# Kernel optimization log

Measured on AMD Instinct MI355X. Metric: run time of the kernel, lower is better.

Reference implementation:

```python
import jax, jax.numpy as jnp
import numpy as np

NGRAM = 2
NUM_HEADS = 16
NUM_BUCKETS = 32
EMBED_DIM = 1024
REAL_T = 512
BSZ = 4


def setup_inputs() -> dict:
    key = jax.random.key(0)
    ks = jax.random.split(key, 10)
    tgt_len = (1 + NGRAM) * REAL_T
    E, H, NB = EMBED_DIM, NUM_HEADS, NUM_BUCKETS
    w = 0.02
    return {
        "query": jax.random.normal(ks[0], (tgt_len, BSZ, E), jnp.float32),
        "self_attn_mask": jnp.zeros((REAL_T, REAL_T), jnp.float32),
        "ngram_mask_matrix": jnp.zeros((NGRAM, REAL_T, 2 * REAL_T), jnp.float32),
        "i_buckets_main_stream": jax.random.randint(ks[1], (BSZ, REAL_T, REAL_T), 0, NB, jnp.int32),
        "i_bucket_relative_stream": jax.random.randint(ks[2], (BSZ, REAL_T, 2 * REAL_T), 0, NB, jnp.int32),
        "in_proj_weight": jax.random.normal(ks[3], (3 * E, E), jnp.float32) * w,
        "in_proj_bias": jnp.zeros((3 * E,), jnp.float32),
        "out_proj_weight": jax.random.normal(ks[4], (E, E), jnp.float32) * w,
        "out_proj_bias": jnp.zeros((E,), jnp.float32),
        "relative_weight": jax.random.normal(ks[5], (NB * H, E), jnp.float32) * w,
        "relative_bias": jnp.zeros((NB * H,), jnp.float32),
    }


def _forward(query, self_attn_mask, ngram_mask_matrix,
             ib_main, ib_rel,
             in_proj_weight, in_proj_bias, out_proj_weight, out_proj_bias,
             relative_weight, relative_bias):
    tgt_len, bsz, E = query.shape
    H, n = NUM_HEADS, NGRAM
    hd = E // H
    nb = relative_weight.shape[0] // H
    T = tgt_len // (1 + n)
    scaling = hd ** -0.5

    # fused qkv projection
    qkv = query @ in_proj_weight.T + in_proj_bias  # [tgt, B, 3E]
    q, k, v = jnp.split(qkv, 3, axis=-1)
    q = q * scaling

    def to_bh(x):  # [tgt, B, E] -> [B*H, tgt, hd]
        return x.reshape(tgt_len, bsz * H, hd).transpose(1, 0, 2)
    q, k, v = to_bh(q), to_bh(k), to_bh(v)

    h_main = query[:T]                                  # [T, B, E]
    h_pred = query[T:].reshape(n, T, bsz, E)            # [n, T, B, E]
    q_main, k_main, v_main = q[:, :T], k[:, :T], v[:, :T]            # [BH, T, hd]
    def pred(x):  # [BH, n*T, hd] -> [n, BH, T, hd]
        return x[:, T:].reshape(bsz * H, n, T, hd).transpose(1, 0, 2, 3)
    q_pred, k_pred, v_pred = pred(q), pred(k), pred(v)

    # ---- main stream ----
    aw_main = jnp.einsum('bth,bsh->bts', q_main, k_main)  # [BH, T, T]
    # relative bias: per-token bucket values gathered by bucket index
    vals_main = h_main.transpose(1, 0, 2) @ relative_weight.T + relative_bias  # [B, T, nb*H]
    vals_main = vals_main.reshape(bsz, T, nb, H).transpose(0, 3, 1, 2)         # [B, H, T, nb]
    ib = jnp.broadcast_to(ib_main[:, None].astype(jnp.int32), (bsz, H, T, T))
    rel_main = jnp.take_along_axis(vals_main, ib, axis=-1).reshape(bsz * H, T, T)
    aw_main = aw_main + rel_main + self_attn_mask[None]
    p_main = jax.nn.softmax(aw_main, axis=-1)
    attn_main = jnp.einsum('bts,bsh->bth', p_main, v_main)  # [BH, T, hd]
    attn_main = attn_main.transpose(1, 0, 2).reshape(T, bsz, E)

    # ---- ngram predict streams ----
    k_ng = jnp.concatenate([jnp.broadcast_to(k_main[None], (n,) + k_main.shape), k_pred], axis=2)  # [n, BH, 2T, hd]
    v_ng = jnp.concatenate([jnp.broadcast_to(v_main[None], (n,) + v_main.shape), v_pred], axis=2)
    aw_ng = jnp.einsum('nbtc,nbsc->nbts', q_pred, k_ng)  # [n, BH, T, 2T]

    vals_ng = h_pred.transpose(0, 2, 1, 3) @ relative_weight.T + relative_bias  # [n, B, T, nb*H]
    vals_ng = vals_ng.reshape(n, bsz, T, nb, H).transpose(0, 1, 4, 2, 3)        # [n, B, H, T, nb]
    ibr = jnp.broadcast_to(ib_rel[None, :, None].astype(jnp.int32), (n, bsz, H, T, 2 * T))
    rel_ng = jnp.take_along_axis(vals_ng, ibr, axis=-1).reshape(n, bsz * H, T, 2 * T)
    aw_ng = aw_ng + rel_ng + ngram_mask_matrix[:, None]
    p_ng = jax.nn.softmax(aw_ng, axis=-1)
    attn_ng = jnp.einsum('nbts,nbsc->nbtc', p_ng, v_ng)  # [n, BH, T, hd]
    attn_ng = attn_ng.transpose(0, 2, 1, 3).reshape(n * T, bsz, E)

    attn = jnp.concatenate([attn_main, attn_ng], axis=0)  # [tgt, B, E]
    return attn @ out_proj_weight.T + out_proj_bias


def reference(query, self_attn_mask, ngram_mask_matrix,
              i_buckets_main_stream, i_bucket_relative_stream,
              in_proj_weight, in_proj_bias, out_proj_weight, out_proj_bias,
              relative_weight, relative_bias):
    return _forward(query, self_attn_mask, ngram_mask_matrix,
                    i_buckets_main_stream, i_bucket_relative_stream,
                    in_proj_weight, in_proj_bias, out_proj_weight, out_proj_bias,
                    relative_weight, relative_bias)
```

## Files before the change

### kernel.cpp

```cpp
#include <hip/hip_runtime.h>

#define TSEQ 512
#define BSZN 4
#define NH 16
#define NBN 32
#define EMB 1024
#define HD 64
#define TGT 1536
#define MROWS 6144

typedef unsigned short ushort_t;
typedef __bf16 bf8 __attribute__((ext_vector_type(8)));
typedef ushort_t u16x8v __attribute__((ext_vector_type(8)));
typedef float f32x4 __attribute__((ext_vector_type(4)));

__device__ __forceinline__ unsigned short f2bf(float f) {
  unsigned int u = __builtin_bit_cast(unsigned int, f);
  u += 0x7fffu + ((u >> 16) & 1u);
  return (unsigned short)(u >> 16);
}

__device__ __forceinline__ float bf2f(unsigned short u) {
  return __builtin_bit_cast(float, (unsigned int)u << 16);
}

__device__ __forceinline__ unsigned int packbf(float a, float b) {
  return (unsigned int)f2bf(a) | ((unsigned int)f2bf(b) << 16);
}

__device__ __forceinline__ void gload16(const void* g, void* l) {
  __builtin_amdgcn_global_load_lds(
      (const __attribute__((address_space(1))) void*)g,
      (__attribute__((address_space(3))) void*)l, 16, 0, 0);
}

__device__ __forceinline__ f32x4 mfma_bf16(bf8 a, bf8 b, f32x4 c) {
  return __builtin_amdgcn_mfma_f32_16x16x32_bf16(a, b, c, 0, 0, 0);
}

__device__ __forceinline__ float lanebcast(float v, int srclane) {
  return __builtin_bit_cast(float,
      __builtin_amdgcn_ds_bpermute(srclane * 4, __builtin_bit_cast(int, v)));
}

__global__ void cvt4_kernel(const float* __restrict__ q, const float* __restrict__ win,
                            const float* __restrict__ wout, const float* __restrict__ wrel,
                            ushort_t* __restrict__ qo, ushort_t* __restrict__ wino,
                            ushort_t* __restrict__ wouto, ushort_t* __restrict__ wrelo) {
  const int i = blockIdx.x * blockDim.x + threadIdx.x;
  const int n0 = 1572864, n1 = 786432, n2 = 262144, n3 = 131072;
  const float* src;
  ushort_t* dst;
  int off;
  if (i < n0) { src = q; dst = qo; off = i; }
  else if (i < n0 + n1) { src = win; dst = wino; off = i - n0; }
  else if (i < n0 + n1 + n2) { src = wout; dst = wouto; off = i - n0 - n1; }
  else if (i < n0 + n1 + n2 + n3) { src = wrel; dst = wrelo; off = i - n0 - n1 - n2; }
  else return;
  const float4 v = reinterpret_cast<const float4*>(src)[off];
  ushort4 o;
  o.x = f2bf(v.x); o.y = f2bf(v.y); o.z = f2bf(v.z); o.w = f2bf(v.w);
  reinterpret_cast<ushort4*>(dst)[off] = o;
}

__global__ void prep_comb_kernel(const int* __restrict__ ibm, const int* __restrict__ ibr,
                                 const float* __restrict__ mm, const float* __restrict__ mng,
                                 unsigned int* __restrict__ cm, unsigned int* __restrict__ cng) {
  const int i = blockIdx.x * blockDim.x + threadIdx.x;
  const int nm = 262144;
  const int nr = 1048576;
  if (i < nm) {
    const int f = i * 4;
    const int4 ib = *reinterpret_cast<const int4*>(ibm + f);
    const float4 mk = *reinterpret_cast<const float4*>(mm + (f & 262143));
    uint4 o;
    o.x = ((unsigned int)f2bf(mk.x) << 16) | ((unsigned int)ib.x & 31u);
    o.y = ((unsigned int)f2bf(mk.y) << 16) | ((unsigned int)ib.y & 31u);
    o.z = ((unsigned int)f2bf(mk.z) << 16) | ((unsigned int)ib.z & 31u);
    o.w = ((unsigned int)f2bf(mk.w) << 16) | ((unsigned int)ib.w & 31u);
    *reinterpret_cast<uint4*>(cm + f) = o;
  } else if (i < nm + nr) {
    const int f = (i - nm) * 4;
    const int ib_off = ((f >> 20) << 19) + (f & 524287);
    const int mk_off = f & 1048575;
    const int4 ib = *reinterpret_cast<const int4*>(ibr + ib_off);
    const float4 mk = *reinterpret_cast<const float4*>(mng + mk_off);
    uint4 o;
    o.x = ((unsigned int)f2bf(mk.x) << 16) | ((unsigned int)ib.x & 31u);
    o.y = ((unsigned int)f2bf(mk.y) << 16) | ((unsigned int)ib.y & 31u);
    o.z = ((unsigned int)f2bf(mk.z) << 16) | ((unsigned int)ib.z & 31u);
    o.w = ((unsigned int)f2bf(mk.w) << 16) | ((unsigned int)ib.w & 31u);
    *reinterpret_cast<uint4*>(cng + f) = o;
  }
}

template <int MODE>
__global__ __launch_bounds__(256) void gemm_bt(
    const ushort_t* __restrict__ A, const ushort_t* __restrict__ B,
    const float* __restrict__ bias, float* __restrict__ Cf,
    ushort_t* __restrict__ Qo, ushort_t* __restrict__ Ko, ushort_t* __restrict__ Vto,
    int M, int N, int K) {
  __shared__ ushort_t lds[16384];
  ushort_t* lA = lds;
  ushort_t* lB = lds + 8192;

  const int tid = threadIdx.x;
  const int lane = tid & 63;
  const int wid = tid >> 6;
  const int l15 = lane & 15, l4 = lane >> 4;
  const int bm = blockIdx.y, bn = blockIdx.x;
  const int wm = (wid >> 1) * 64, wn = (wid & 1) * 64;

  f32x4 acc[4][4] = {};

  const int r8 = tid >> 3;
  const int c8 = ((tid & 7) ^ (r8 & 7)) * 8;
  const ushort_t* Ag = A + (size_t)(bm * 128 + r8) * K + c8;
  const ushort_t* Bg = B + (size_t)(bn * 128 + r8) * K + c8;
  ushort_t* lAp = lA + tid * 8;
  ushort_t* lBp = lB + tid * 8;

  for (int kt = 0; kt < K; kt += 64) {
    __syncthreads();
#pragma unroll
    for (int i = 0; i < 4; ++i) {
      gload16(Ag + (size_t)i * 32 * K + kt, lAp + i * 2048);
      gload16(Bg + (size_t)i * 32 * K + kt, lBp + i * 2048);
    }
    __syncthreads();
#pragma unroll
    for (int k0 = 0; k0 < 2; ++k0) {
      bf8 af[4], bv[4];
#pragma unroll
      for (int mi = 0; mi < 4; ++mi) {
        const int row = wm + mi * 16 + l15;
        const int slot = (k0 * 4 + l4) ^ (row & 7);
        af[mi] = *reinterpret_cast<const bf8*>(lA + row * 64 + slot * 8);
      }
#pragma unroll
      for (int ni = 0; ni < 4; ++ni) {
        const int row = wn + ni * 16 + l15;
        const int slot = (k0 * 4 + l4) ^ (row & 7);
        bv[ni] = *reinterpret_cast<const bf8*>(lB + row * 64 + slot * 8);
      }
#pragma unroll
      for (int mi = 0; mi < 4; ++mi)
#pragma unroll
        for (int ni = 0; ni < 4; ++ni)
          acc[mi][ni] = mfma_bf16(af[mi], bv[ni], acc[mi][ni]);
    }
  }

  if (MODE == 0 && bn >= 16) {
    __syncthreads();
    char* tb = reinterpret_cast<char*>(lds);
#pragma unroll
    for (int ni = 0; ni < 4; ++ni) {
      const int colloc = wn + ni * 16 + l15;
      const float bc = bias[bn * 128 + colloc];
      const unsigned int swz = (colloc & 7) << 4;
#pragma unroll
      for (int mi = 0; mi < 4; ++mi) {
        const int t_loc = (wm >> 2) + mi * 4 + l4;
        f32x4 v = acc[mi][ni];
#pragma unroll
        for (int r = 0; r < 4; ++r) {
          const int byteoff = colloc * 256 + ((r * 64 + t_loc * 2) ^ swz);
          *reinterpret_cast<ushort_t*>(tb + byteoff) = f2bf(v[r] + bc);
        }
      }
    }
    __syncthreads();
    const int tglob0 = bm * 32;
#pragma unroll
    for (int p = 0; p < 2; ++p) {
      const int pair = wid * 2 + p;
      const int bb = pair >> 1;
      const int hl = pair & 1;
      const int hh = (bn - 16) * 2 + hl;
      const int bh = bb * NH + hh;
      const int tch = lane & 3;
#pragma unroll
      for (int ii = 0; ii < 4; ++ii) {
        const int dloc = ii * 16 + (lane >> 2);
        const int colloc = hl * 64 + dloc;
        const int byteoff = colloc * 256 + ((bb * 64 + tch * 16) ^ ((colloc & 7) << 4));
        const u16x8v val = *reinterpret_cast<const u16x8v*>(tb + byteoff);
        *reinterpret_cast<u16x8v*>(
            Vto + ((size_t)bh * HD + dloc) * TGT + tglob0 + tch * 8) = val;
      }
    }
    return;
  }

#pragma unroll
  for (int ni = 0; ni < 4; ++ni) {
    const int col = bn * 128 + wn + ni * 16 + l15;
    const float bc = bias[col];
#pragma unroll
    for (int mi = 0; mi < 4; ++mi) {
      const int row0 = bm * 128 + wm + mi * 16 + l4 * 4;
      f32x4 v = acc[mi][ni];
#pragma unroll
      for (int r = 0; r < 4; ++r) {
        const int row = row0 + r;
        float val = v[r] + bc;
        if (MODE == 0) {
          const int part = col >> 10;
          const int cc = col & 1023;
          const int h = cc >> 6, d = cc & 63;
          const int t = row >> 2, bb = row & 3;
          const int bh = bb * NH + h;
          if (part == 0) {
            Qo[((size_t)bh * TGT + t) * HD + d] = f2bf(val * 0.125f);
          } else {
            Ko[((size_t)bh * TGT + t) * HD + d] = f2bf(val);
          }
        } else if (MODE == 3) {
          const int hh = col & 15, nb = col >> 4;
          const int qg = row >> 2, bb2 = row & 3;
          Qo[(((size_t)(bb2 * NH + hh)) * TGT + qg) * NBN + nb] = f2bf(val);
        } else {
          Cf[(size_t)row * N + col] = val;
        }
      }
    }
  }
}

__global__ __launch_bounds__(256, 3) void attn_kernel(
    const ushort_t* __restrict__ Q, const ushort_t* __restrict__ Kb,
    const ushort_t* __restrict__ Vt, const ushort_t* __restrict__ VMh,
    const unsigned int* __restrict__ comb_main, const unsigned int* __restrict__ comb_ng,
    ushort_t* __restrict__ AT) {
  __shared__ unsigned char kbuf[8192];
  __shared__ unsigned char vbuf[8192];
  __shared__ ushort_t vmt[4][1024];
  __shared__ unsigned int pbl[4][1152];

  const int tid = threadIdx.x;
  const int lane = tid & 63, wid = tid >> 6;
  const int l15 = lane & 15, l4 = lane >> 4;

  const int n = blockIdx.x;
  const int xcd = n & 7;
  const int b = xcd >> 1;
  const int idx = (xcd & 1) * 96 + (n >> 3);
  const int h = idx / 12;
  const int rem = idx - h * 12;
  const int z = rem >> 2;
  const int blk = rem & 3;
  const int g = (z == 0) ? 0 : z - 1;
  const int bh = b * NH + h;
  const int t0 = blk * 128 + wid * 32;
  const int qrow0 = (z == 0) ? t0 : TSEQ + g * TSEQ + t0;
  const int nsb = (z == 0) ? 8 : 16;

  gload16(VMh + ((size_t)bh * TGT + qrow0 + (lane >> 2)) * NBN + (lane & 3) * 8,
          (ushort_t*)vmt[wid] + lane * 8);
  gload16(VMh + ((size_t)bh * TGT + qrow0 + 16 + (lane >> 2)) * NBN + (lane & 3) * 8,
          (ushort_t*)vmt[wid] + 512 + lane * 8);

  bf8 qf[2][2];
#pragma unroll
  for (int th = 0; th < 2; ++th)
#pragma unroll
    for (int hf = 0; hf < 2; ++hf)
      qf[th][hf] = *reinterpret_cast<const bf8*>(
          &Q[((size_t)bh * TGT + qrow0 + th * 16 + l15) * HD + hf * 32 + l4 * 8]);

  const unsigned int* cb[2];
  {
    const unsigned int* cbase = (z == 0)
        ? comb_main + (size_t)b * TSEQ * TSEQ
        : comb_ng + (size_t)(b * 2 + g) * TSEQ * (2 * TSEQ);
    const int sstr = (z == 0) ? TSEQ : 2 * TSEQ;
    cb[0] = cbase + (size_t)(t0 + l15) * sstr;
    cb[1] = cbase + (size_t)(t0 + 16 + l15) * sstr;
  }

  float m_run[2] = {-1e30f, -1e30f};
  float l_run[2] = {0.f, 0.f};
  f32x4 oacc[2][4] = {};

  const int r8 = lane >> 3;
  const int swzs = ((lane & 7) ^ r8) << 4;
  const int swzr = (l15 & 7) << 4;

  for (int sb = 0; sb < nsb; ++sb) {
    const int srow0 = (sb < 8) ? sb * 64 : TSEQ + g * TSEQ + (sb - 8) * 64;
    const int scol = sb * 64;

    __syncthreads();
    {
      const ushort_t* ks = Kb + ((size_t)bh * TGT + srow0 + wid * 16 + r8) * HD + (swzs >> 1);
      gload16(ks, kbuf + wid * 2048 + lane * 16);
      gload16(ks + 8 * HD, kbuf + wid * 2048 + 1024 + lane * 16);
      const ushort_t* vs = Vt + ((size_t)bh * HD + wid * 16 + r8) * TGT + srow0 + (swzs >> 1);
      gload16(vs, vbuf + wid * 2048 + lane * 16);
      gload16(vs + 8 * TGT, vbuf + wid * 2048 + 1024 + lane * 16);
    }
    __syncthreads();

    bf8 kf[4][2];
#pragma unroll
    for (int j = 0; j < 4; ++j) {
      const int row = j * 16 + l15;
      kf[j][0] = *reinterpret_cast<const bf8*>(kbuf + row * 128 + ((l4 * 16) ^ swzr));
      kf[j][1] = *reinterpret_cast<const bf8*>(kbuf + row * 128 + ((64 + l4 * 16) ^ swzr));
    }

#pragma unroll
    for (int th = 0; th < 2; ++th) {
      const unsigned int* cwp = cb[th] + scol + l4 * 4;
      const uint4 c0 = *reinterpret_cast<const uint4*>(cwp);
      const uint4 c1 = *reinterpret_cast<const uint4*>(cwp + 16);
      const uint4 c2 = *reinterpret_cast<const uint4*>(cwp + 32);
      const uint4 c3 = *reinterpret_cast<const uint4*>(cwp + 48);
      const unsigned int cwa[4][4] = {{c0.x, c0.y, c0.z, c0.w},
                                      {c1.x, c1.y, c1.z, c1.w},
                                      {c2.x, c2.y, c2.z, c2.w},
                                      {c3.x, c3.y, c3.z, c3.w}};
      f32x4 st[4];
#pragma unroll
      for (int j = 0; j < 4; ++j) {
        f32x4 s4 = {};
        s4 = mfma_bf16(kf[j][0], qf[th][0], s4);
        s4 = mfma_bf16(kf[j][1], qf[th][1], s4);
        st[j] = s4;
      }
      const ushort_t* vrow = vmt[wid] + (th * 16 + l15) * 32;
      float vals[4][4];
      float mx = -1e30f;
#pragma unroll
      for (int j = 0; j < 4; ++j) {
#pragma unroll
        for (int r = 0; r < 4; ++r) {
          const unsigned int w = cwa[j][r];
          const float v = st[j][r] + bf2f((ushort_t)(w >> 16)) + bf2f(vrow[w & 31u]);
          vals[j][r] = v;
          mx = fmaxf(mx, v);
        }
      }
      mx = fmaxf(mx, __shfl_xor(mx, 16));
      mx = fmaxf(mx, __shfl_xor(mx, 32));
      const float oldm = m_run[th];
      const float newm = fmaxf(oldm, mx);
      const float fct = (oldm <= -1e30f) ? 0.f : __expf(oldm - newm);
      float lsum = 0.f;
#pragma unroll
      for (int j = 0; j < 4; ++j) {
        const float p0 = __expf(vals[j][0] - newm);
        const float p1 = __expf(vals[j][1] - newm);
        const float p2 = __expf(vals[j][2] - newm);
        const float p3 = __expf(vals[j][3] - newm);
        lsum += (p0 + p1) + (p2 + p3);
        pbl[wid][th * 576 + l15 * 36 + j * 8 + l4 * 2 + 0] = packbf(p0, p1);
        pbl[wid][th * 576 + l15 * 36 + j * 8 + l4 * 2 + 1] = packbf(p2, p3);
      }
      lsum += __shfl_xor(lsum, 16);
      lsum += __shfl_xor(lsum, 32);
      l_run[th] = l_run[th] * fct + lsum;
      m_run[th] = newm;

      f32x4 rs;
      rs[0] = lanebcast(fct, l4 * 4 + 0);
      rs[1] = lanebcast(fct, l4 * 4 + 1);
      rs[2] = lanebcast(fct, l4 * 4 + 2);
      rs[3] = lanebcast(fct, l4 * 4 + 3);
#pragma unroll
      for (int dt = 0; dt < 4; ++dt) oacc[th][dt] *= rs;

      const ushort_t* pbase = reinterpret_cast<const ushort_t*>(&pbl[wid][th * 576]);
#pragma unroll
      for (int k32 = 0; k32 < 2; ++k32) {
        const bf8 pa = *reinterpret_cast<const bf8*>(pbase + l15 * 72 + k32 * 32 + l4 * 8);
#pragma unroll
        for (int dt = 0; dt < 4; ++dt) {
          const bf8 vb = *reinterpret_cast<const bf8*>(
              vbuf + (dt * 16 + l15) * 128 + ((k32 * 64 + l4 * 16) ^ swzr));
          oacc[th][dt] = mfma_bf16(pa, vb, oacc[th][dt]);
        }
      }
    }
  }

#pragma unroll
  for (int th = 0; th < 2; ++th) {
    const float linv = 1.f / l_run[th];
    f32x4 bs;
    bs[0] = lanebcast(linv, l4 * 4 + 0);
    bs[1] = lanebcast(linv, l4 * 4 + 1);
    bs[2] = lanebcast(linv, l4 * 4 + 2);
    bs[3] = lanebcast(linv, l4 * 4 + 3);
#pragma unroll
    for (int dt = 0; dt < 4; ++dt) {
#pragma unroll
      for (int r = 0; r < 4; ++r) {
        const int tout = qrow0 + th * 16 + l4 * 4 + r;
        AT[((size_t)tout * BSZN + b) * EMB + h * HD + dt * 16 + l15] =
            f2bf(oacc[th][dt][r] * bs[r]);
      }
    }
  }
}

extern "C" void kernel_launch(void* const* d_in, const int* in_sizes, int n_in,
                              void* d_out, int out_size, void* d_ws, size_t ws_size,
                              hipStream_t stream) {
  const float* query     = (const float*)d_in[0];
  const float* mask_main = (const float*)d_in[1];
  const float* mask_ng   = (const float*)d_in[2];
  const int*   ib_main   = (const int*)d_in[3];
  const int*   ib_rel    = (const int*)d_in[4];
  const float* w_in      = (const float*)d_in[5];
  const float* b_in      = (const float*)d_in[6];
  const float* w_out     = (const float*)d_in[7];
  const float* b_out     = (const float*)d_in[8];
  const float* w_rel     = (const float*)d_in[9];
  const float* b_rel     = (const float*)d_in[10];
  float* out = (float*)d_out;

  ushort_t* qbf    = (ushort_t*)d_ws;
  ushort_t* winbf  = qbf + 6291456;
  ushort_t* woutbf = winbf + 3145728;
  ushort_t* relwbf = woutbf + 1048576;
  ushort_t* Qb     = relwbf + 524288;
  ushort_t* Kbuf   = Qb + 6291456;
  ushort_t* Vtb    = Kbuf + 6291456;
  ushort_t* VMh    = Vtb + 6291456;
  unsigned int* comb_main = (unsigned int*)(VMh + 3145728);
  unsigned int* comb_ng   = comb_main + 1048576;
  ushort_t* AT     = qbf;

  {
    const int total4 = 1572864 + 786432 + 262144 + 131072;
    cvt4_kernel<<<(total4 + 255) / 256, 256, 0, stream>>>(query, w_in, w_out, w_rel,
                                                          qbf, winbf, woutbf, relwbf);
  }
  prep_comb_kernel<<<(262144 + 1048576) / 256, 256, 0, stream>>>(
      ib_main, ib_rel, mask_main, mask_ng, comb_main, comb_ng);

  gemm_bt<0><<<dim3(24, 48), 256, 0, stream>>>(qbf, winbf, b_in, nullptr,
                                               Qb, Kbuf, Vtb, MROWS, 3072, 1024);
  gemm_bt<3><<<dim3(4, 48), 256, 0, stream>>>(qbf, relwbf, b_rel, nullptr,
                                              VMh, nullptr, nullptr, MROWS, 512, 1024);
  attn_kernel<<<768, 256, 0, stream>>>(Qb, Kbuf, Vtb, VMh, comb_main, comb_ng, AT);
  gemm_bt<2><<<dim3(8, 48), 256, 0, stream>>>(AT, woutbf, b_out, out,
                                              nullptr, nullptr, nullptr, MROWS, 1024, 1024);
}
```

Measured before the change: 217.6 us.

## Double-buffer K/V tiles, use exp2 softmax with lazy rescale, merge prep kernels

The attention kernel now double-buffers its K/V LDS tiles, prefetching the next block while computing the current one, so each iteration needs one barrier instead of two. The log2(e) factor is folded into Q scaling, the relative-bucket values and the masks, so the softmax can use exp2f. Accumulator rescaling is skipped unless the running max rises by more than 8. The P staging buffer is shrunk and swizzled, stored with vector writes, and bf16 conversion uses native casts. The two preprocessing kernels are merged into one launch. The lazy rescale lets exponentials reach up to 2^8 before bf16 packing, which carries some accuracy risk, and the extra LDS buffers may reduce occupancy.

Measured after the change: 212.9 us. 2.1% less time.

```diff
diff --git a/kernel.cpp b/kernel.cpp
--- a/kernel.cpp
+++ b/kernel.cpp
@@ -8,16 +8,17 @@
 #define HD 64
 #define TGT 1536
 #define MROWS 6144
+#define LOG2E 1.44269504088896f
 
 typedef unsigned short ushort_t;
 typedef __bf16 bf8 __attribute__((ext_vector_type(8)));
+typedef __bf16 bf2_t __attribute__((ext_vector_type(2)));
 typedef ushort_t u16x8v __attribute__((ext_vector_type(8)));
+typedef unsigned int u32x2 __attribute__((ext_vector_type(2)));
 typedef float f32x4 __attribute__((ext_vector_type(4)));
 
 __device__ __forceinline__ unsigned short f2bf(float f) {
-  unsigned int u = __builtin_bit_cast(unsigned int, f);
-  u += 0x7fffu + ((u >> 16) & 1u);
-  return (unsigned short)(u >> 16);
+  return __builtin_bit_cast(unsigned short, (__bf16)f);
 }
 
 __device__ __forceinline__ float bf2f(unsigned short u) {
@@ -25,7 +26,10 @@
 }
 
 __device__ __forceinline__ unsigned int packbf(float a, float b) {
-  return (unsigned int)f2bf(a) | ((unsigned int)f2bf(b) << 16);
+  bf2_t t;
+  t[0] = (__bf16)a;
+  t[1] = (__bf16)b;
+  return __builtin_bit_cast(unsigned int, t);
 }
 
 __device__ __forceinline__ void gload16(const void* g, void* l) {
@@ -43,53 +47,50 @@
       __builtin_amdgcn_ds_bpermute(srclane * 4, __builtin_bit_cast(int, v)));
 }
 
-__global__ void cvt4_kernel(const float* __restrict__ q, const float* __restrict__ win,
-                            const float* __restrict__ wout, const float* __restrict__ wrel,
-                            ushort_t* __restrict__ qo, ushort_t* __restrict__ wino,
-                            ushort_t* __restrict__ wouto, ushort_t* __restrict__ wrelo) {
+__global__ void prep_all_kernel(const float* __restrict__ q, const float* __restrict__ win,
+                                const float* __restrict__ wout, const float* __restrict__ wrel,
+                                const int* __restrict__ ibm, const int* __restrict__ ibr,
+                                const float* __restrict__ mm, const float* __restrict__ mng,
+                                ushort_t* __restrict__ qo, ushort_t* __restrict__ wino,
+                                ushort_t* __restrict__ wouto, ushort_t* __restrict__ wrelo,
+                                unsigned int* __restrict__ cm, unsigned int* __restrict__ cng) {
   const int i = blockIdx.x * blockDim.x + threadIdx.x;
   const int n0 = 1572864, n1 = 786432, n2 = 262144, n3 = 131072;
-  const float* src;
-  ushort_t* dst;
-  int off;
-  if (i < n0) { src = q; dst = qo; off = i; }
-  else if (i < n0 + n1) { src = win; dst = wino; off = i - n0; }
-  else if (i < n0 + n1 + n2) { src = wout; dst = wouto; off = i - n0 - n1; }
-  else if (i < n0 + n1 + n2 + n3) { src = wrel; dst = wrelo; off = i - n0 - n1 - n2; }
-  else return;
-  const float4 v = reinterpret_cast<const float4*>(src)[off];
-  ushort4 o;
-  o.x = f2bf(v.x); o.y = f2bf(v.y); o.z = f2bf(v.z); o.w = f2bf(v.w);
-  reinterpret_cast<ushort4*>(dst)[off] = o;
-}
-
-__global__ void prep_comb_kernel(const int* __restrict__ ibm, const int* __restrict__ ibr,
-                                 const float* __restrict__ mm, const float* __restrict__ mng,
-                                 unsigned int* __restrict__ cm, unsigned int* __restrict__ cng) {
-  const int i = blockIdx.x * blockDim.x + threadIdx.x;
-  const int nm = 262144;
-  const int nr = 1048576;
-  if (i < nm) {
-    const int f = i * 4;
+  const int ncvt = n0 + n1 + n2 + n3;
+  const int nm = 262144, nr = 1048576;
+  if (i < ncvt) {
+    const float* src;
+    ushort_t* dst;
+    int off;
+    if (i < n0) { src = q; dst = qo; off = i; }
+    else if (i < n0 + n1) { src = win; dst = wino; off = i - n0; }
+    else if (i < n0 + n1 + n2) { src = wout; dst = wouto; off = i - n0 - n1; }
+    else { src = wrel; dst = wrelo; off = i - n0 - n1 - n2; }
+    const float4 v = reinterpret_cast<const float4*>(src)[off];
+    ushort4 o;
+    o.x = f2bf(v.x); o.y = f2bf(v.y); o.z = f2bf(v.z); o.w = f2bf(v.w);
+    reinterpret_cast<ushort4*>(dst)[off] = o;
+  } else if (i < ncvt + nm) {
+    const int f = (i - ncvt) * 4;
     const int4 ib = *reinterpret_cast<const int4*>(ibm + f);
     const float4 mk = *reinterpret_cast<const float4*>(mm + (f & 262143));
     uint4 o;
-    o.x = ((unsigned int)f2bf(mk.x) << 16) | ((unsigned int)ib.x & 31u);
-    o.y = ((unsigned int)f2bf(mk.y) << 16) | ((unsigned int)ib.y & 31u);
-    o.z = ((unsigned int)f2bf(mk.z) << 16) | ((unsigned int)ib.z & 31u);
-    o.w = ((unsigned int)f2bf(mk.w) << 16) | ((unsigned int)ib.w & 31u);
+    o.x = ((unsigned int)f2bf(mk.x * LOG2E) << 16) | ((unsigned int)ib.x & 31u);
+    o.y = ((unsigned int)f2bf(mk.y * LOG2E) << 16) | ((unsigned int)ib.y & 31u);
+    o.z = ((unsigned int)f2bf(mk.z * LOG2E) << 16) | ((unsigned int)ib.z & 31u);
+    o.w = ((unsigned int)f2bf(mk.w * LOG2E) << 16) | ((unsigned int)ib.w & 31u);
     *reinterpret_cast<uint4*>(cm + f) = o;
-  } else if (i < nm + nr) {
-    const int f = (i - nm) * 4;
+  } else if (i < ncvt + nm + nr) {
+    const int f = (i - ncvt - nm) * 4;
     const int ib_off = ((f >> 20) << 19) + (f & 524287);
     const int mk_off = f & 1048575;
     const int4 ib = *reinterpret_cast<const int4*>(ibr + ib_off);
     const float4 mk = *reinterpret_cast<const float4*>(mng + mk_off);
     uint4 o;
-    o.x = ((unsigned int)f2bf(mk.x) << 16) | ((unsigned int)ib.x & 31u);
-    o.y = ((unsigned int)f2bf(mk.y) << 16) | ((unsigned int)ib.y & 31u);
-    o.z = ((unsigned int)f2bf(mk.z) << 16) | ((unsigned int)ib.z & 31u);
-    o.w = ((unsigned int)f2bf(mk.w) << 16) | ((unsigned int)ib.w & 31u);
+    o.x = ((unsigned int)f2bf(mk.x * LOG2E) << 16) | ((unsigned int)ib.x & 31u);
+    o.y = ((unsigned int)f2bf(mk.y * LOG2E) << 16) | ((unsigned int)ib.y & 31u);
+    o.z = ((unsigned int)f2bf(mk.z * LOG2E) << 16) | ((unsigned int)ib.z & 31u);
+    o.w = ((unsigned int)f2bf(mk.w * LOG2E) << 16) | ((unsigned int)ib.w & 31u);
     *reinterpret_cast<uint4*>(cng + f) = o;
   }
 }
@@ -212,14 +213,14 @@
           const int t = row >> 2, bb = row & 3;
           const int bh = bb * NH + h;
           if (part == 0) {
-            Qo[((size_t)bh * TGT + t) * HD + d] = f2bf(val * 0.125f);
+            Qo[((size_t)bh * TGT + t) * HD + d] = f2bf(val * (0.125f * LOG2E));
           } else {
             Ko[((size_t)bh * TGT + t) * HD + d] = f2bf(val);
           }
         } else if (MODE == 3) {
           const int hh = col & 15, nb = col >> 4;
           const int qg = row >> 2, bb2 = row & 3;
-          Qo[(((size_t)(bb2 * NH + hh)) * TGT + qg) * NBN + nb] = f2bf(val);
+          Qo[(((size_t)(bb2 * NH + hh)) * TGT + qg) * NBN + nb] = f2bf(val * LOG2E);
         } else {
           Cf[(size_t)row * N + col] = val;
         }
@@ -233,10 +234,10 @@
     const ushort_t* __restrict__ Vt, const ushort_t* __restrict__ VMh,
     const unsigned int* __restrict__ comb_main, const unsigned int* __restrict__ comb_ng,
     ushort_t* __restrict__ AT) {
-  __shared__ unsigned char kbuf[8192];
-  __shared__ unsigned char vbuf[8192];
+  __shared__ unsigned char kbuf[2][8192];
+  __shared__ unsigned char vbuf[2][8192];
   __shared__ ushort_t vmt[4][1024];
-  __shared__ unsigned int pbl[4][1152];
+  __shared__ unsigned int pbl[4][512];
 
   const int tid = threadIdx.x;
   const int lane = tid & 63, wid = tid >> 6;
@@ -286,28 +287,36 @@
   const int r8 = lane >> 3;
   const int swzs = ((lane & 7) ^ r8) << 4;
   const int swzr = (l15 & 7) << 4;
-
+  const int swz2 = (l15 & 7) << 2;
+
+  auto stage = [&](int sb, int bf) {
+    const int srow0 = (sb < 8) ? sb * 64 : TSEQ + g * TSEQ + (sb - 8) * 64;
+    const ushort_t* ks = Kb + ((size_t)bh * TGT + srow0 + wid * 16 + r8) * HD + (swzs >> 1);
+    gload16(ks, &kbuf[bf][wid * 2048 + lane * 16]);
+    gload16(ks + 8 * HD, &kbuf[bf][wid * 2048 + 1024 + lane * 16]);
+    const ushort_t* vs = Vt + ((size_t)bh * HD + wid * 16 + r8) * TGT + srow0 + (swzs >> 1);
+    gload16(vs, &vbuf[bf][wid * 2048 + lane * 16]);
+    gload16(vs + 8 * TGT, &vbuf[bf][wid * 2048 + 1024 + lane * 16]);
+  };
+
+  stage(0, 0);
+  asm volatile("s_waitcnt vmcnt(0)" ::: "memory");
+  __builtin_amdgcn_s_barrier();
+
+  int cur = 0;
   for (int sb = 0; sb < nsb; ++sb) {
-    const int srow0 = (sb < 8) ? sb * 64 : TSEQ + g * TSEQ + (sb - 8) * 64;
     const int scol = sb * 64;
-
-    __syncthreads();
-    {
-      const ushort_t* ks = Kb + ((size_t)bh * TGT + srow0 + wid * 16 + r8) * HD + (swzs >> 1);
-      gload16(ks, kbuf + wid * 2048 + lane * 16);
-      gload16(ks + 8 * HD, kbuf + wid * 2048 + 1024 + lane * 16);
-      const ushort_t* vs = Vt + ((size_t)bh * HD + wid * 16 + r8) * TGT + srow0 + (swzs >> 1);
-      gload16(vs, vbuf + wid * 2048 + lane * 16);
-      gload16(vs + 8 * TGT, vbuf + wid * 2048 + 1024 + lane * 16);
-    }
-    __syncthreads();
+    if (sb + 1 < nsb) stage(sb + 1, cur ^ 1);
+
+    const unsigned char* kb = kbuf[cur];
+    const unsigned char* vbb = vbuf[cur];
 
     bf8 kf[4][2];
 #pragma unroll
     for (int j = 0; j < 4; ++j) {
       const int row = j * 16 + l15;
-      kf[j][0] = *reinterpret_cast<const bf8*>(kbuf + row * 128 + ((l4 * 16) ^ swzr));
-      kf[j][1] = *reinterpret_cast<const bf8*>(kbuf + row * 128 + ((64 + l4 * 16) ^ swzr));
+      kf[j][0] = *reinterpret_cast<const bf8*>(kb + row * 128 + ((l4 * 16) ^ swzr));
+      kf[j][1] = *reinterpret_cast<const bf8*>(kb + row * 128 + ((64 + l4 * 16) ^ swzr));
     }
 
 #pragma unroll
@@ -337,52 +346,65 @@
 #pragma unroll
         for (int r = 0; r < 4; ++r) {
           const unsigned int w = cwa[j][r];
-          const float v = st[j][r] + bf2f((ushort_t)(w >> 16)) + bf2f(vrow[w & 31u]);
+          const float v = st[j][r] + __builtin_bit_cast(float, w & 0xffff0000u) +
+                          bf2f(vrow[w & 31u]);
           vals[j][r] = v;
           mx = fmaxf(mx, v);
         }
       }
       mx = fmaxf(mx, __shfl_xor(mx, 16));
       mx = fmaxf(mx, __shfl_xor(mx, 32));
+
       const float oldm = m_run[th];
-      const float newm = fmaxf(oldm, mx);
-      const float fct = (oldm <= -1e30f) ? 0.f : __expf(oldm - newm);
+      if (!__all(mx - oldm <= 8.f)) {
+        const float newm = fmaxf(oldm, mx);
+        const float fct = (oldm <= -1e30f) ? 0.f : exp2f(oldm - newm);
+        f32x4 rs;
+        rs[0] = lanebcast(fct, l4 * 4 + 0);
+        rs[1] = lanebcast(fct, l4 * 4 + 1);
+        rs[2] = lanebcast(fct, l4 * 4 + 2);
+        rs[3] = lanebcast(fct, l4 * 4 + 3);
+#pragma unroll
+        for (int dt = 0; dt < 4; ++dt) oacc[th][dt] *= rs;
+        l_run[th] *= fct;
+        m_run[th] = newm;
+      }
+      const float mref = m_run[th];
+
       float lsum = 0.f;
 #pragma unroll
       for (int j = 0; j < 4; ++j) {
-        const float p0 = __expf(vals[j][0] - newm);
-        const float p1 = __expf(vals[j][1] - newm);
-        const float p2 = __expf(vals[j][2] - newm);
-        const float p3 = __expf(vals[j][3] - newm);
+        const float p0 = exp2f(vals[j][0] - mref);
+        const float p1 = exp2f(vals[j][1] - mref);
+        const float p2 = exp2f(vals[j][2] - mref);
+        const float p3 = exp2f(vals[j][3] - mref);
         lsum += (p0 + p1) + (p2 + p3);
-        pbl[wid][th * 576 + l15 * 36 + j * 8 + l4 * 2 + 0] = packbf(p0, p1);
-        pbl[wid][th * 576 + l15 * 36 + j * 8 + l4 * 2 + 1] = packbf(p2, p3);
+        u32x2 pw;
+        pw[0] = packbf(p0, p1);
+        pw[1] = packbf(p2, p3);
+        *reinterpret_cast<u32x2*>(&pbl[wid][l15 * 32 + ((j * 8 + l4 * 2) ^ swz2)]) = pw;
       }
       lsum += __shfl_xor(lsum, 16);
       lsum += __shfl_xor(lsum, 32);
-      l_run[th] = l_run[th] * fct + lsum;
-      m_run[th] = newm;
-
-      f32x4 rs;
-      rs[0] = lanebcast(fct, l4 * 4 + 0);
-      rs[1] = lanebcast(fct, l4 * 4 + 1);
-      rs[2] = lanebcast(fct, l4 * 4 + 2);
-      rs[3] = lanebcast(fct, l4 * 4 + 3);
-#pragma unroll
-      for (int dt = 0; dt < 4; ++dt) oacc[th][dt] *= rs;
-
-      const ushort_t* pbase = reinterpret_cast<const ushort_t*>(&pbl[wid][th * 576]);
+      l_run[th] += lsum;
+
+      const unsigned char* pbase = reinterpret_cast<const unsigned char*>(&pbl[wid][0]);
 #pragma unroll
       for (int k32 = 0; k32 < 2; ++k32) {
-        const bf8 pa = *reinterpret_cast<const bf8*>(pbase + l15 * 72 + k32 * 32 + l4 * 8);
+        const bf8 pa = *reinterpret_cast<const bf8*>(
+            pbase + l15 * 128 + ((k32 * 64 + l4 * 16) ^ swzr));
 #pragma unroll
         for (int dt = 0; dt < 4; ++dt) {
           const bf8 vb = *reinterpret_cast<const bf8*>(
-              vbuf + (dt * 16 + l15) * 128 + ((k32 * 64 + l4 * 16) ^ swzr));
+              vbb + (dt * 16 + l15) * 128 + ((k32 * 64 + l4 * 16) ^ swzr));
           oacc[th][dt] = mfma_bf16(pa, vb, oacc[th][dt]);
         }
       }
     }
+
+    asm volatile("s_waitcnt vmcnt(0)" ::: "memory");
+    __builtin_amdgcn_s_barrier();
+    cur ^= 1;
   }
 
 #pragma unroll
@@ -434,12 +456,11 @@
   ushort_t* AT     = qbf;
 
   {
-    const int total4 = 1572864 + 786432 + 262144 + 131072;
-    cvt4_kernel<<<(total4 + 255) / 256, 256, 0, stream>>>(query, w_in, w_out, w_rel,
-                                                          qbf, winbf, woutbf, relwbf);
-  }
-  prep_comb_kernel<<<(262144 + 1048576) / 256, 256, 0, stream>>>(
-      ib_main, ib_rel, mask_main, mask_ng, comb_main, comb_ng);
+    const int total = 2752512 + 262144 + 1048576;
+    prep_all_kernel<<<(total + 255) / 256, 256, 0, stream>>>(
+        query, w_in, w_out, w_rel, ib_main, ib_rel, mask_main, mask_ng,
+        qbf, winbf, woutbf, relwbf, comb_main, comb_ng);
+  }
 
   gemm_bt<0><<<dim3(24, 48), 256, 0, stream>>>(qbf, winbf, b_in, nullptr,
                                                Qb, Kbuf, Vtb, MROWS, 3072, 1024);
```
